# Kernel tuning notes

Measured on AMD Instinct MI355X. Metric: run time of the kernel, lower is better.

The kernel has to match this reference:

```python
import jax, jax.numpy as jnp
import numpy as np

B, T, H, M = 262144, 100, 32, 64  # batch, seq_len, gru_hidden, mlp_hidden
NSCAL = 4                          # weight_norm, grad_norm, loss_current, step_progress
LR_MIN, LR_MAX = 1e-08, 100.0


def setup_inputs() -> dict:
    key = jax.random.key(0)
    ks = jax.random.split(key, 11)
    lecun = lambda k, shape, fan_in: (jax.random.normal(k, shape, jnp.float32) / np.sqrt(fan_in)).astype(jnp.float32)
    return {
        "loss_history": jax.random.normal(ks[0], (B, T), jnp.float32),
        "weight_norm": jax.random.uniform(ks[1], (B,), jnp.float32),
        "grad_norm": jax.random.uniform(ks[2], (B,), jnp.float32),
        "loss_current": jax.random.uniform(ks[3], (B,), jnp.float32),
        "step_progress": jax.random.uniform(ks[4], (B,), jnp.float32),
        # GRU params: input denses (no bias) and hidden denses (bias), gates stacked [r|z|n]
        "Wi": lecun(ks[5], (1, 3 * H), 1),      # input size is 1 (loss scalar)
        "Wh": lecun(ks[6], (H, 3 * H), H),
        "bh": jnp.zeros((3 * H,), jnp.float32),
        # MLP head
        "W1": lecun(ks[7], (NSCAL + H, M), NSCAL + H),
        "b1": jnp.zeros((M,), jnp.float32),
        "W2": lecun(ks[8], (M, M), M),
        "b2": jnp.zeros((M,), jnp.float32),
        "W3": lecun(ks[9], (M, 1), M),
        "b3": jnp.zeros((1,), jnp.float32),
    }


def reference(loss_history, weight_norm, grad_norm, loss_current, step_progress,
              Wi, Wh, bh, W1, b1, W2, b2, W3, b3):
    xs = loss_history.T  # [T, B]

    def step(h, x):  # h: [B, H], x: [B]
        gi = x[:, None] * Wi[0]          # [B, 3H] (input dim is 1, no bias)
        gh = h @ Wh + bh                 # [B, 3H]
        gi_r, gi_z, gi_n = jnp.split(gi, 3, axis=1)
        gh_r, gh_z, gh_n = jnp.split(gh, 3, axis=1)
        r = jax.nn.sigmoid(gi_r + gh_r)
        z = jax.nn.sigmoid(gi_z + gh_z)
        n = jnp.tanh(gi_n + r * gh_n)    # flax GRUCell: r gates (Wh_n h + b_n)
        return (1.0 - z) * n + z * h, None

    h0 = jnp.zeros((loss_history.shape[0], H), loss_history.dtype)
    h, _ = jax.lax.scan(step, h0, xs)    # final carry [B, H]

    scal = jnp.stack([weight_norm, grad_norm, loss_current, step_progress], axis=1)  # [B, 4]
    x = jnp.concatenate([scal, h], axis=1)          # [B, 4+H]
    x = jax.nn.relu(x @ W1 + b1)
    x = jax.nn.relu(x @ W2 + b2)
    logit = (x @ W3 + b3)[:, 0]                     # [B]
    return jax.nn.sigmoid(logit) * (LR_MAX - LR_MIN) + LR_MIN
```

## Files before the change

kernel.cpp:

```cpp
#include <hip/hip_runtime.h>

namespace {

typedef __attribute__((ext_vector_type(8))) short short8;
typedef __attribute__((ext_vector_type(4))) float floatx4;

constexpr int T = 100;
constexpr int H = 32;
constexpr int M = 64;
constexpr float L2E = 1.4426950408889634f;

__device__ __forceinline__ float fast_exp2(float x) { return __builtin_amdgcn_exp2f(x); }
__device__ __forceinline__ float fast_rcp(float x)  { return __builtin_amdgcn_rcpf(x); }
__device__ __forceinline__ float fast_sigmoid(float x) {
  return fast_rcp(1.0f + fast_exp2(-L2E * x));
}

__device__ __forceinline__ unsigned short bf16_rne(float f) {
  unsigned u = __float_as_uint(f);
  return (unsigned short)((u + 0x7FFFu + ((u >> 16) & 1u)) >> 16);
}
__device__ __forceinline__ float bf16_f32(unsigned short s) {
  return __uint_as_float(((unsigned)s) << 16);
}

__global__ __launch_bounds__(256, 2) void lrpred_kernel(
    const float* __restrict__ loss_history,
    const float* __restrict__ weight_norm,
    const float* __restrict__ grad_norm,
    const float* __restrict__ loss_current,
    const float* __restrict__ step_progress,
    const float* __restrict__ Wi,
    const float* __restrict__ Wh,
    const float* __restrict__ bh,
    const float* __restrict__ W1,
    const float* __restrict__ b1,
    const float* __restrict__ W2,
    const float* __restrict__ b2,
    const float* __restrict__ W3,
    const float* __restrict__ b3,
    float* __restrict__ out,
    int B)
{
  const int lane = threadIdx.x & 63;
  const int wid  = threadIdx.x >> 6;
  const int c = lane & 15;
  const int p = lane >> 4;
  const int blockBase = blockIdx.x * 256;
  const int waveBase  = blockBase + wid * 64;

  short8 wHi[6], wLo[6];
#pragma unroll
  for (int mt = 0; mt < 6; ++mt) {
    const float sc = (mt < 4) ? -L2E : (2.0f * L2E);
    short8 hi, lo;
#pragma unroll
    for (int e = 0; e < 8; ++e) {
      const int k = (e >> 2) * 16 + 4 * p + (e & 3);
      const float w = Wh[k * (3 * H) + mt * 16 + c] * sc;
      const unsigned short h16 = bf16_rne(w);
      hi[e] = (short)h16;
      lo[e] = (short)bf16_rne(w - bf16_f32(h16));
    }
    wHi[mt] = hi;
    wLo[mt] = lo;
  }

  float wiR[8], wiZ[8], wiN[8], bhR[8], bhZ[8], bhN[8];
#pragma unroll
  for (int e = 0; e < 8; ++e) {
    const int j = (e >> 2) * 16 + 4 * p + (e & 3);
    wiR[e] = Wi[j]          * -L2E;          bhR[e] = bh[j]          * -L2E;
    wiZ[e] = Wi[H + j]      * -L2E;          bhZ[e] = bh[H + j]      * -L2E;
    wiN[e] = Wi[2 * H + j]  * (2.0f * L2E);  bhN[e] = bh[2 * H + j]  * (2.0f * L2E);
  }

  float hs[4][8];
#pragma unroll
  for (int nt = 0; nt < 4; ++nt)
#pragma unroll
    for (int e = 0; e < 8; ++e) hs[nt][e] = 0.0f;

  const float* xp0 = loss_history + (size_t)(waveBase +  0 + c) * T;
  const float* xp1 = loss_history + (size_t)(waveBase + 16 + c) * T;
  const float* xp2 = loss_history + (size_t)(waveBase + 32 + c) * T;
  const float* xp3 = loss_history + (size_t)(waveBase + 48 + c) * T;
  float xv[4], xn[4];
  xv[0] = xp0[0]; xv[1] = xp1[0]; xv[2] = xp2[0]; xv[3] = xp3[0];

#pragma unroll 1
  for (int t = 0; t < T; ++t) {
    if (t + 1 < T) {
      xn[0] = xp0[t + 1]; xn[1] = xp1[t + 1]; xn[2] = xp2[t + 1]; xn[3] = xp3[t + 1];
    }
#pragma unroll
    for (int nt = 0; nt < 4; ++nt) {
      short8 bHi, bLo;
#pragma unroll
      for (int e = 0; e < 8; ++e) {
        const float v = hs[nt][e];
        const unsigned short h16 = bf16_rne(v);
        bHi[e] = (short)h16;
        bLo[e] = (short)bf16_rne(v - bf16_f32(h16));
      }
      floatx4 aR0 = {bhR[0], bhR[1], bhR[2], bhR[3]};
      floatx4 aR1 = {bhR[4], bhR[5], bhR[6], bhR[7]};
      floatx4 aZ0 = {bhZ[0], bhZ[1], bhZ[2], bhZ[3]};
      floatx4 aZ1 = {bhZ[4], bhZ[5], bhZ[6], bhZ[7]};
      floatx4 aN0 = {bhN[0], bhN[1], bhN[2], bhN[3]};
      floatx4 aN1 = {bhN[4], bhN[5], bhN[6], bhN[7]};
      aR0 = __builtin_amdgcn_mfma_f32_16x16x32_bf16(wHi[0], bHi, aR0, 0, 0, 0);
      aR0 = __builtin_amdgcn_mfma_f32_16x16x32_bf16(wLo[0], bHi, aR0, 0, 0, 0);
      aR0 = __builtin_amdgcn_mfma_f32_16x16x32_bf16(wHi[0], bLo, aR0, 0, 0, 0);
      aR1 = __builtin_amdgcn_mfma_f32_16x16x32_bf16(wHi[1], bHi, aR1, 0, 0, 0);
      aR1 = __builtin_amdgcn_mfma_f32_16x16x32_bf16(wLo[1], bHi, aR1, 0, 0, 0);
      aR1 = __builtin_amdgcn_mfma_f32_16x16x32_bf16(wHi[1], bLo, aR1, 0, 0, 0);
      aZ0 = __builtin_amdgcn_mfma_f32_16x16x32_bf16(wHi[2], bHi, aZ0, 0, 0, 0);
      aZ0 = __builtin_amdgcn_mfma_f32_16x16x32_bf16(wLo[2], bHi, aZ0, 0, 0, 0);
      aZ0 = __builtin_amdgcn_mfma_f32_16x16x32_bf16(wHi[2], bLo, aZ0, 0, 0, 0);
      aZ1 = __builtin_amdgcn_mfma_f32_16x16x32_bf16(wHi[3], bHi, aZ1, 0, 0, 0);
      aZ1 = __builtin_amdgcn_mfma_f32_16x16x32_bf16(wLo[3], bHi, aZ1, 0, 0, 0);
      aZ1 = __builtin_amdgcn_mfma_f32_16x16x32_bf16(wHi[3], bLo, aZ1, 0, 0, 0);
      aN0 = __builtin_amdgcn_mfma_f32_16x16x32_bf16(wHi[4], bHi, aN0, 0, 0, 0);
      aN0 = __builtin_amdgcn_mfma_f32_16x16x32_bf16(wLo[4], bHi, aN0, 0, 0, 0);
      aN0 = __builtin_amdgcn_mfma_f32_16x16x32_bf16(wHi[4], bLo, aN0, 0, 0, 0);
      aN1 = __builtin_amdgcn_mfma_f32_16x16x32_bf16(wHi[5], bHi, aN1, 0, 0, 0);
      aN1 = __builtin_amdgcn_mfma_f32_16x16x32_bf16(wLo[5], bHi, aN1, 0, 0, 0);
      aN1 = __builtin_amdgcn_mfma_f32_16x16x32_bf16(wHi[5], bLo, aN1, 0, 0, 0);

      const float xb = xv[nt];
#pragma unroll
      for (int e = 0; e < 8; ++e) {
        const float ar = (e < 4) ? aR0[e & 3] : aR1[e & 3];
        const float az = (e < 4) ? aZ0[e & 3] : aZ1[e & 3];
        const float an = (e < 4) ? aN0[e & 3] : aN1[e & 3];
        const float r  = fast_rcp(1.0f + fast_exp2(fmaf(xb, wiR[e], ar)));
        const float z  = fast_rcp(1.0f + fast_exp2(fmaf(xb, wiZ[e], az)));
        const float pn = fmaf(r, an, xb * wiN[e]);
        const float n  = fmaf(-2.0f, fast_rcp(fast_exp2(pn) + 1.0f), 1.0f);
        hs[nt][e] = fmaf(z, hs[nt][e] - n, n);
      }
    }
    xv[0] = xn[0]; xv[1] = xn[1]; xv[2] = xn[2]; xv[3] = xn[3];
  }

  __shared__ float hsh[256][36];
#pragma unroll
  for (int nt = 0; nt < 4; ++nt) {
    const int row = wid * 64 + nt * 16 + c;
#pragma unroll
    for (int q = 0; q < 2; ++q) {
      floatx4 v = {hs[nt][q * 4 + 0], hs[nt][q * 4 + 1],
                   hs[nt][q * 4 + 2], hs[nt][q * 4 + 3]};
      *(floatx4*)&hsh[row][q * 16 + 4 * p] = v;
    }
  }
  __syncthreads();

  const int b = blockBase + threadIdx.x;
  const float s0 = weight_norm[b];
  const float s1 = grad_norm[b];
  const float s2 = loss_current[b];
  const float s3 = step_progress[b];

  float a1[M];
#pragma unroll
  for (int m = 0; m < M; ++m) a1[m] = b1[m];
#pragma unroll
  for (int m = 0; m < M; ++m) a1[m] = fmaf(s0, W1[0 * M + m], a1[m]);
#pragma unroll
  for (int m = 0; m < M; ++m) a1[m] = fmaf(s1, W1[1 * M + m], a1[m]);
#pragma unroll
  for (int m = 0; m < M; ++m) a1[m] = fmaf(s2, W1[2 * M + m], a1[m]);
#pragma unroll
  for (int m = 0; m < M; ++m) a1[m] = fmaf(s3, W1[3 * M + m], a1[m]);
#pragma unroll
  for (int k = 0; k < H; ++k) {
    const float hk = hsh[threadIdx.x][k];
#pragma unroll
    for (int m = 0; m < M; ++m)
      a1[m] = fmaf(hk, W1[(4 + k) * M + m], a1[m]);
  }
#pragma unroll
  for (int m = 0; m < M; ++m) a1[m] = fmaxf(a1[m], 0.0f);

  float logit = b3[0];
#pragma unroll
  for (int hf = 0; hf < 2; ++hf) {
    float a2[32];
#pragma unroll
    for (int m = 0; m < 32; ++m) a2[m] = b2[hf * 32 + m];
#pragma unroll
    for (int i = 0; i < M; ++i) {
      const float xi = a1[i];
#pragma unroll
      for (int m = 0; m < 32; ++m)
        a2[m] = fmaf(xi, W2[i * M + hf * 32 + m], a2[m]);
    }
#pragma unroll
    for (int m = 0; m < 32; ++m)
      logit = fmaf(fmaxf(a2[m], 0.0f), W3[hf * 32 + m], logit);
  }

  out[b] = fmaf(fast_sigmoid(logit), 100.0f - 1e-8f, 1e-8f);
}

}

extern "C" void kernel_launch(void* const* d_in, const int* in_sizes, int n_in,
                              void* d_out, int out_size, void* d_ws, size_t ws_size,
                              hipStream_t stream) {
  const float* loss_history  = (const float*)d_in[0];
  const float* weight_norm   = (const float*)d_in[1];
  const float* grad_norm     = (const float*)d_in[2];
  const float* loss_current  = (const float*)d_in[3];
  const float* step_progress = (const float*)d_in[4];
  const float* Wi            = (const float*)d_in[5];
  const float* Wh            = (const float*)d_in[6];
  const float* bh            = (const float*)d_in[7];
  const float* W1            = (const float*)d_in[8];
  const float* b1            = (const float*)d_in[9];
  const float* W2            = (const float*)d_in[10];
  const float* b2            = (const float*)d_in[11];
  const float* W3            = (const float*)d_in[12];
  const float* b3            = (const float*)d_in[13];
  float* out = (float*)d_out;

  const int B = in_sizes[1];
  const int grid = B / 256;
  lrpred_kernel<<<grid, 256, 0, stream>>>(
      loss_history, weight_norm, grad_norm, loss_current, step_progress,
      Wi, Wh, bh, W1, b1, W2, b2, W3, b3, out, B);
}
```

Baseline: 964.2 us.

## Fold GRU input and bias terms into an extra MFMA and use packed bf16 conversion

Folds the input-times-Wi contribution for the r/z gates and the hidden bias into an extra MFMA per gate tile, built from a small auxiliary A/B fragment carrying split bf16 values of x, Wi and bh. The bias-initialised accumulators and per-element FMAs are removed. Hi/lo bf16 splitting of h now uses the hardware packed v_cvt_pk_bf16_f32 instruction instead of manual integer rounding. The MFMA order is regrouped by gate so independent accumulators interleave, and launch bounds are raised to 3 blocks per CU. This adds 6 MFMAs per tile and may raise register pressure under the tighter occupancy target.

```diff
diff --git a/kernel.cpp b/kernel.cpp
--- a/kernel.cpp
+++ b/kernel.cpp
@@ -4,6 +4,7 @@
 
 typedef __attribute__((ext_vector_type(8))) short short8;
 typedef __attribute__((ext_vector_type(4))) float floatx4;
+typedef __attribute__((ext_vector_type(4))) unsigned uint4v;
 
 constexpr int T = 100;
 constexpr int H = 32;
@@ -23,8 +24,13 @@
 __device__ __forceinline__ float bf16_f32(unsigned short s) {
   return __uint_as_float(((unsigned)s) << 16);
 }
-
-__global__ __launch_bounds__(256, 2) void lrpred_kernel(
+__device__ __forceinline__ unsigned cvt_pk_bf16(float a, float b) {
+  unsigned r;
+  asm("v_cvt_pk_bf16_f32 %0, %1, %2" : "=v"(r) : "v"(a), "v"(b));
+  return r;
+}
+
+__global__ __launch_bounds__(256, 3) void lrpred_kernel(
     const float* __restrict__ loss_history,
     const float* __restrict__ weight_norm,
     const float* __restrict__ grad_norm,
@@ -46,6 +52,7 @@
   const int wid  = threadIdx.x >> 6;
   const int c = lane & 15;
   const int p = lane >> 4;
+  const bool isp0 = (p == 0);
   const int blockBase = blockIdx.x * 256;
   const int waveBase  = blockBase + wid * 64;
 
@@ -66,14 +73,35 @@
     wLo[mt] = lo;
   }
 
-  float wiR[8], wiZ[8], wiN[8], bhR[8], bhZ[8], bhN[8];
+  short8 wAux[6];
+#pragma unroll
+  for (int mt = 0; mt < 6; ++mt) {
+    const float sc = (mt < 4) ? -L2E : (2.0f * L2E);
+    const int g = mt * 16 + c;
+    const float wi_s = (mt < 4) ? Wi[g] * sc : 0.0f;
+    const float bh_s = bh[g] * sc;
+    const unsigned short wi_hi = bf16_rne(wi_s);
+    const unsigned short wi_lo = bf16_rne(wi_s - bf16_f32(wi_hi));
+    const unsigned short bh_hi = bf16_rne(bh_s);
+    const unsigned short bh_lo = bf16_rne(bh_s - bf16_f32(bh_hi));
+    short8 a = {0, 0, 0, 0, 0, 0, 0, 0};
+    if (p == 0) {
+      a[0] = (short)wi_hi; a[1] = (short)wi_hi;
+      a[2] = (short)bh_hi; a[3] = (short)wi_lo;
+    } else if (p == 1) {
+      a[0] = (short)bh_lo;
+    }
+    wAux[mt] = a;
+  }
+
+  float wiN[8];
 #pragma unroll
   for (int e = 0; e < 8; ++e) {
     const int j = (e >> 2) * 16 + 4 * p + (e & 3);
-    wiR[e] = Wi[j]          * -L2E;          bhR[e] = bh[j]          * -L2E;
-    wiZ[e] = Wi[H + j]      * -L2E;          bhZ[e] = bh[H + j]      * -L2E;
-    wiN[e] = Wi[2 * H + j]  * (2.0f * L2E);  bhN[e] = bh[2 * H + j]  * (2.0f * L2E);
-  }
+    wiN[e] = Wi[2 * H + j] * (2.0f * L2E);
+  }
+
+  const unsigned w0_rest = (p == 1) ? 0x00003F80u : 0u;
 
   float hs[4][8];
 #pragma unroll
@@ -88,6 +116,8 @@
   float xv[4], xn[4];
   xv[0] = xp0[0]; xv[1] = xp1[0]; xv[2] = xp2[0]; xv[3] = xp3[0];
 
+  const floatx4 z4 = {0.0f, 0.0f, 0.0f, 0.0f};
+
 #pragma unroll 1
   for (int t = 0; t < T; ++t) {
     if (t + 1 < T) {
@@ -95,47 +125,62 @@
     }
 #pragma unroll
     for (int nt = 0; nt < 4; ++nt) {
-      short8 bHi, bLo;
-#pragma unroll
-      for (int e = 0; e < 8; ++e) {
-        const float v = hs[nt][e];
-        const unsigned short h16 = bf16_rne(v);
-        bHi[e] = (short)h16;
-        bLo[e] = (short)bf16_rne(v - bf16_f32(h16));
-      }
-      floatx4 aR0 = {bhR[0], bhR[1], bhR[2], bhR[3]};
-      floatx4 aR1 = {bhR[4], bhR[5], bhR[6], bhR[7]};
-      floatx4 aZ0 = {bhZ[0], bhZ[1], bhZ[2], bhZ[3]};
-      floatx4 aZ1 = {bhZ[4], bhZ[5], bhZ[6], bhZ[7]};
-      floatx4 aN0 = {bhN[0], bhN[1], bhN[2], bhN[3]};
-      floatx4 aN1 = {bhN[4], bhN[5], bhN[6], bhN[7]};
+      unsigned hw0 = cvt_pk_bf16(hs[nt][0], hs[nt][1]);
+      unsigned hw1 = cvt_pk_bf16(hs[nt][2], hs[nt][3]);
+      unsigned hw2 = cvt_pk_bf16(hs[nt][4], hs[nt][5]);
+      unsigned hw3 = cvt_pk_bf16(hs[nt][6], hs[nt][7]);
+      unsigned lw0 = cvt_pk_bf16(hs[nt][0] - __uint_as_float(hw0 << 16),
+                                 hs[nt][1] - __uint_as_float(hw0 & 0xFFFF0000u));
+      unsigned lw1 = cvt_pk_bf16(hs[nt][2] - __uint_as_float(hw1 << 16),
+                                 hs[nt][3] - __uint_as_float(hw1 & 0xFFFF0000u));
+      unsigned lw2 = cvt_pk_bf16(hs[nt][4] - __uint_as_float(hw2 << 16),
+                                 hs[nt][5] - __uint_as_float(hw2 & 0xFFFF0000u));
+      unsigned lw3 = cvt_pk_bf16(hs[nt][6] - __uint_as_float(hw3 << 16),
+                                 hs[nt][7] - __uint_as_float(hw3 & 0xFFFF0000u));
+      short8 bHi = __builtin_bit_cast(short8, (uint4v){hw0, hw1, hw2, hw3});
+      short8 bLo = __builtin_bit_cast(short8, (uint4v){lw0, lw1, lw2, lw3});
+
+      const float xb = xv[nt];
+      unsigned u0 = cvt_pk_bf16(xb, 0.0f);
+      float xlo = xb - __uint_as_float(u0 << 16);
+      unsigned w0p0 = cvt_pk_bf16(xb, xlo);
+      unsigned w1p0 = (u0 << 16) | 0x3F80u;
+      unsigned bw0 = isp0 ? w0p0 : w0_rest;
+      unsigned bw1 = isp0 ? w1p0 : 0u;
+      short8 bAux = __builtin_bit_cast(short8, (uint4v){bw0, bw1, 0u, 0u});
+
+      floatx4 aR0 = __builtin_amdgcn_mfma_f32_16x16x32_bf16(wAux[0], bAux, z4, 0, 0, 0);
+      floatx4 aR1 = __builtin_amdgcn_mfma_f32_16x16x32_bf16(wAux[1], bAux, z4, 0, 0, 0);
+      floatx4 aZ0 = __builtin_amdgcn_mfma_f32_16x16x32_bf16(wAux[2], bAux, z4, 0, 0, 0);
+      floatx4 aZ1 = __builtin_amdgcn_mfma_f32_16x16x32_bf16(wAux[3], bAux, z4, 0, 0, 0);
+      floatx4 aN0 = __builtin_amdgcn_mfma_f32_16x16x32_bf16(wAux[4], bAux, z4, 0, 0, 0);
+      floatx4 aN1 = __builtin_amdgcn_mfma_f32_16x16x32_bf16(wAux[5], bAux, z4, 0, 0, 0);
+      aR0 = __builtin_amdgcn_mfma_f32_16x16x32_bf16(wHi[0], bLo, aR0, 0, 0, 0);
+      aR1 = __builtin_amdgcn_mfma_f32_16x16x32_bf16(wHi[1], bLo, aR1, 0, 0, 0);
+      aZ0 = __builtin_amdgcn_mfma_f32_16x16x32_bf16(wHi[2], bLo, aZ0, 0, 0, 0);
+      aZ1 = __builtin_amdgcn_mfma_f32_16x16x32_bf16(wHi[3], bLo, aZ1, 0, 0, 0);
+      aN0 = __builtin_amdgcn_mfma_f32_16x16x32_bf16(wHi[4], bLo, aN0, 0, 0, 0);
+      aN1 = __builtin_amdgcn_mfma_f32_16x16x32_bf16(wHi[5], bLo, aN1, 0, 0, 0);
+      aR0 = __builtin_amdgcn_mfma_f32_16x16x32_bf16(wLo[0], bHi, aR0, 0, 0, 0);
+      aR1 = __builtin_amdgcn_mfma_f32_16x16x32_bf16(wLo[1], bHi, aR1, 0, 0, 0);
+      aZ0 = __builtin_amdgcn_mfma_f32_16x16x32_bf16(wLo[2], bHi, aZ0, 0, 0, 0);
+      aZ1 = __builtin_amdgcn_mfma_f32_16x16x32_bf16(wLo[3], bHi, aZ1, 0, 0, 0);
+      aN0 = __builtin_amdgcn_mfma_f32_16x16x32_bf16(wLo[4], bHi, aN0, 0, 0, 0);
+      aN1 = __builtin_amdgcn_mfma_f32_16x16x32_bf16(wLo[5], bHi, aN1, 0, 0, 0);
       aR0 = __builtin_amdgcn_mfma_f32_16x16x32_bf16(wHi[0], bHi, aR0, 0, 0, 0);
-      aR0 = __builtin_amdgcn_mfma_f32_16x16x32_bf16(wLo[0], bHi, aR0, 0, 0, 0);
-      aR0 = __builtin_amdgcn_mfma_f32_16x16x32_bf16(wHi[0], bLo, aR0, 0, 0, 0);
       aR1 = __builtin_amdgcn_mfma_f32_16x16x32_bf16(wHi[1], bHi, aR1, 0, 0, 0);
-      aR1 = __builtin_amdgcn_mfma_f32_16x16x32_bf16(wLo[1], bHi, aR1, 0, 0, 0);
-      aR1 = __builtin_amdgcn_mfma_f32_16x16x32_bf16(wHi[1], bLo, aR1, 0, 0, 0);
       aZ0 = __builtin_amdgcn_mfma_f32_16x16x32_bf16(wHi[2], bHi, aZ0, 0, 0, 0);
-      aZ0 = __builtin_amdgcn_mfma_f32_16x16x32_bf16(wLo[2], bHi, aZ0, 0, 0, 0);
-      aZ0 = __builtin_amdgcn_mfma_f32_16x16x32_bf16(wHi[2], bLo, aZ0, 0, 0, 0);
       aZ1 = __builtin_amdgcn_mfma_f32_16x16x32_bf16(wHi[3], bHi, aZ1, 0, 0, 0);
-      aZ1 = __builtin_amdgcn_mfma_f32_16x16x32_bf16(wLo[3], bHi, aZ1, 0, 0, 0);
-      aZ1 = __builtin_amdgcn_mfma_f32_16x16x32_bf16(wHi[3], bLo, aZ1, 0, 0, 0);
       aN0 = __builtin_amdgcn_mfma_f32_16x16x32_bf16(wHi[4], bHi, aN0, 0, 0, 0);
-      aN0 = __builtin_amdgcn_mfma_f32_16x16x32_bf16(wLo[4], bHi, aN0, 0, 0, 0);
-      aN0 = __builtin_amdgcn_mfma_f32_16x16x32_bf16(wHi[4], bLo, aN0, 0, 0, 0);
       aN1 = __builtin_amdgcn_mfma_f32_16x16x32_bf16(wHi[5], bHi, aN1, 0, 0, 0);
-      aN1 = __builtin_amdgcn_mfma_f32_16x16x32_bf16(wLo[5], bHi, aN1, 0, 0, 0);
-      aN1 = __builtin_amdgcn_mfma_f32_16x16x32_bf16(wHi[5], bLo, aN1, 0, 0, 0);
-
-      const float xb = xv[nt];
+
 #pragma unroll
       for (int e = 0; e < 8; ++e) {
         const float ar = (e < 4) ? aR0[e & 3] : aR1[e & 3];
         const float az = (e < 4) ? aZ0[e & 3] : aZ1[e & 3];
         const float an = (e < 4) ? aN0[e & 3] : aN1[e & 3];
-        const float r  = fast_rcp(1.0f + fast_exp2(fmaf(xb, wiR[e], ar)));
-        const float z  = fast_rcp(1.0f + fast_exp2(fmaf(xb, wiZ[e], az)));
+        const float r  = fast_rcp(1.0f + fast_exp2(ar));
+        const float z  = fast_rcp(1.0f + fast_exp2(az));
         const float pn = fmaf(r, an, xb * wiN[e]);
         const float n  = fmaf(-2.0f, fast_rcp(fast_exp2(pn) + 1.0f), 1.0f);
         hs[nt][e] = fmaf(z, hs[nt][e] - n, n);
```

After: 931.5 us. 1.04x faster.
